# Kernel optimization log

Measured on AMD Instinct MI355X. Metric: run time of the kernel, lower is better.

## Reference

```python
import jax, jax.numpy as jnp
import numpy as np
from jax import lax

TAGSET = 9
START, STOP = 7, 8
HID = 500  # hidden_dim // 2 per direction
BERT_H = 768
T = 8192
NEG = -10000.0


def setup_inputs() -> dict:
    key = jax.random.key(0)
    ks = jax.random.split(key, 16)
    trans = jax.random.normal(ks[13], (TAGSET, TAGSET), jnp.float32)
    trans = trans.at[START, :].set(NEG).at[:, STOP].set(NEG)
    return {
        "embeddings": jax.random.normal(ks[0], (T, BERT_H), jnp.float32),
        "w_ih_f": jax.random.normal(ks[1], (4 * HID, BERT_H), jnp.float32) * 0.05,
        "w_hh_f": jax.random.normal(ks[2], (4 * HID, HID), jnp.float32) * 0.05,
        "b_ih_f": jax.random.normal(ks[3], (4 * HID,), jnp.float32) * 0.05,
        "b_hh_f": jax.random.normal(ks[4], (4 * HID,), jnp.float32) * 0.05,
        "w_ih_b": jax.random.normal(ks[5], (4 * HID, BERT_H), jnp.float32) * 0.05,
        "w_hh_b": jax.random.normal(ks[6], (4 * HID, HID), jnp.float32) * 0.05,
        "b_ih_b": jax.random.normal(ks[7], (4 * HID,), jnp.float32) * 0.05,
        "b_hh_b": jax.random.normal(ks[8], (4 * HID,), jnp.float32) * 0.05,
        "h0": jax.random.normal(ks[9], (2, HID), jnp.float32),
        "c0": jax.random.normal(ks[10], (2, HID), jnp.float32),
        "w_tag": jax.random.normal(ks[11], (TAGSET, 2 * HID), jnp.float32) * 0.05,
        "b_tag": jax.random.normal(ks[12], (TAGSET,), jnp.float32) * 0.05,
        "transitions": trans,
    }


def _lstm_dir(x, w_ih, w_hh, b_ih, b_hh, h0, c0, reverse):
    # pre-compute input projections for all timesteps: [T, 4H]
    xproj = x @ w_ih.T + b_ih + b_hh

    def step(carry, xp):
        h, c = carry
        g = xp + w_hh @ h  # [4H]
        i, f, gg, o = jnp.split(g, 4)  # torch gate order: i, f, g, o
        i, f, o = jax.nn.sigmoid(i), jax.nn.sigmoid(f), jax.nn.sigmoid(o)
        c = f * c + i * jnp.tanh(gg)
        h = o * jnp.tanh(c)
        return (h, c), h

    _, hs = lax.scan(step, (h0, c0), xproj, reverse=reverse)
    return hs  # [T, H]


def _viterbi(feats, transitions):
    init = jnp.full((TAGSET,), NEG, feats.dtype).at[START].set(0.0)

    def step(fv, feat):
        scores = fv[None, :] + transitions  # [next_tag, prev_tag]
        bptr = jnp.argmax(scores, axis=1)
        fv_new = jnp.max(scores, axis=1) + feat
        return fv_new, bptr

    fv, bptrs = lax.scan(step, init, feats)  # bptrs: [T, TAGSET]
    terminal = fv + transitions[STOP]
    best_last = jnp.argmax(terminal)
    path_score = terminal[best_last]

    def back(tag, bp):
        return bp[tag], tag  # emit tag at time t, carry tag at t-1

    _, path = lax.scan(back, best_last, bptrs, reverse=True)
    return path_score, path


def reference(embeddings, w_ih_f, w_hh_f, b_ih_f, b_hh_f,
              w_ih_b, w_hh_b, b_ih_b, b_hh_b,
              h0, c0, w_tag, b_tag, transitions):
    h_fwd = _lstm_dir(embeddings, w_ih_f, w_hh_f, b_ih_f, b_hh_f, h0[0], c0[0], False)
    h_bwd = _lstm_dir(embeddings, w_ih_b, w_hh_b, b_ih_b, b_hh_b, h0[1], c0[1], True)
    lstm_out = jnp.concatenate([h_fwd, h_bwd], axis=-1)  # [T, 1000]
    feats = lstm_out @ w_tag.T + b_tag  # [T, TAGSET]
    score, path = _viterbi(feats, transitions)
    return score, path
```

## Files before the change

### kernel.cpp

```cpp
#include <hip/hip_runtime.h>
#include <hip/hip_bf16.h>
#include <math.h>

constexpr int TSEQ = 8192;
constexpr int BH   = 768;
constexpr int HID  = 500;
constexpr int H4   = 2000;
constexpr int NTAG = 9;
constexpr int START_TAG = 7;
constexpr int STOP_TAG  = 8;
constexpr float NEGV = -10000.0f;

constexpr int NWG = 32;
constexpr int UPW = 16;

constexpr size_t XP_OFF = 0;
constexpr size_t XP_SZ  = (size_t)2 * TSEQ * H4;
constexpr size_t HS_OFF = XP_OFF + XP_SZ;
constexpr size_t HS_SZ  = (size_t)2 * TSEQ * HID;
constexpr size_t FT_OFF = HS_OFF + HS_SZ;
constexpr size_t FT_SZ  = (size_t)TSEQ * NTAG;
constexpr size_t BUF_OFF = FT_OFF + FT_SZ;

__device__ __forceinline__ float wave_reduce_sum(float v) {
    int x;
    x = __builtin_amdgcn_update_dpp(0, __float_as_int(v), 0x111, 0xF, 0xF, true);
    v += __int_as_float(x);
    x = __builtin_amdgcn_update_dpp(0, __float_as_int(v), 0x112, 0xF, 0xF, true);
    v += __int_as_float(x);
    x = __builtin_amdgcn_update_dpp(0, __float_as_int(v), 0x114, 0xF, 0xF, true);
    v += __int_as_float(x);
    x = __builtin_amdgcn_update_dpp(0, __float_as_int(v), 0x118, 0xF, 0xF, true);
    v += __int_as_float(x);
    x = __builtin_amdgcn_update_dpp(0, __float_as_int(v), 0x142, 0xF, 0xF, true);
    v += __int_as_float(x);
    x = __builtin_amdgcn_update_dpp(0, __float_as_int(v), 0x143, 0xF, 0xF, true);
    v += __int_as_float(x);
    return v;
}

__global__ __launch_bounds__(256) void xproj_gemm(
    const float* __restrict__ A,
    const float* __restrict__ Wf, const float* __restrict__ Wb,
    const float* __restrict__ bif, const float* __restrict__ bhf,
    const float* __restrict__ bib, const float* __restrict__ bhb,
    float* __restrict__ out)
{
    __shared__ __align__(16) float As[8 * 128];
    __shared__ __align__(16) float Bs[8 * 128];

    const int bx = blockIdx.x, by = blockIdx.y;
    const int d    = by >> 4;
    const int col0 = (by & 15) << 7;
    const int row0 = bx << 7;
    const float* W  = d ? Wb : Wf;
    const float* bi = d ? bib : bif;
    const float* bh = d ? bhb : bhf;

    const int tid = threadIdx.x;
    const int tx = tid & 15, ty = tid >> 4;

    float acc[8][8];
#pragma unroll
    for (int i = 0; i < 8; ++i)
#pragma unroll
        for (int j = 0; j < 8; ++j) acc[i][j] = 0.f;

    const int lm = tid >> 1;
    const int lk = (tid & 1) << 2;
    const float* Ap = A + (size_t)(row0 + lm) * BH + lk;
    const int wcol = col0 + lm;
    const bool wok = wcol < H4;
    const float* Wp = W + (size_t)(wok ? wcol : 0) * BH + lk;

    for (int k0 = 0; k0 < BH; k0 += 8) {
        const float4 av = *(const float4*)(Ap + k0);
        float4 bv = make_float4(0.f, 0.f, 0.f, 0.f);
        if (wok) bv = *(const float4*)(Wp + k0);
        __syncthreads();
        As[(lk + 0) * 128 + lm] = av.x;
        As[(lk + 1) * 128 + lm] = av.y;
        As[(lk + 2) * 128 + lm] = av.z;
        As[(lk + 3) * 128 + lm] = av.w;
        Bs[(lk + 0) * 128 + lm] = bv.x;
        Bs[(lk + 1) * 128 + lm] = bv.y;
        Bs[(lk + 2) * 128 + lm] = bv.z;
        Bs[(lk + 3) * 128 + lm] = bv.w;
        __syncthreads();
#pragma unroll
        for (int kk = 0; kk < 8; ++kk) {
            float a[8], b[8];
            *(float4*)&a[0] = *(const float4*)&As[kk * 128 + ty * 8];
            *(float4*)&a[4] = *(const float4*)&As[kk * 128 + ty * 8 + 4];
            *(float4*)&b[0] = *(const float4*)&Bs[kk * 128 + tx * 8];
            *(float4*)&b[4] = *(const float4*)&Bs[kk * 128 + tx * 8 + 4];
#pragma unroll
            for (int i = 0; i < 8; ++i)
#pragma unroll
                for (int j = 0; j < 8; ++j)
                    acc[i][j] = fmaf(a[i], b[j], acc[i][j]);
        }
    }

#pragma unroll
    for (int i = 0; i < 8; ++i) {
        const int r = row0 + ty * 8 + i;
#pragma unroll
        for (int j = 0; j < 8; ++j) {
            const int cc = col0 + tx * 8 + j;
            if (cc < H4)
                out[((size_t)d * TSEQ + r) * H4 + cc] = acc[i][j] + bi[cc] + bh[cc];
        }
    }
}

__global__ __launch_bounds__(512) void lstm_rec(
    const float* __restrict__ whhf, const float* __restrict__ whhb,
    const float* __restrict__ h0, const float* __restrict__ c0,
    const float* __restrict__ xproj_all, float* __restrict__ hseq_all,
    unsigned long long* bufbase)
{
    __shared__ __align__(16) float wlds[64 * 512];
    __shared__ __align__(16) float hs[512];
    __shared__ float gparts[64];

    const int bx = blockIdx.x;
    const int d = bx & 1, w = bx >> 1;
    const float* whh = d ? whhb : whhf;
    const float* xproj = xproj_all + (size_t)d * TSEQ * H4;
    float* hseq = hseq_all + (size_t)d * TSEQ * HID;
    unsigned long long* bufd = bufbase + d * 1024;

    const int j0 = w * UPW;
    int nu = HID - j0; if (nu > UPW) nu = UPW; if (nu < 0) nu = 0;
    const int tid = threadIdx.x, l = tid & 63, wv = tid >> 6;

    for (int idx = tid; idx < 64 * 512; idx += 512) {
        const int r = idx >> 9, c = idx & 511;
        const int g = r >> 4, u = r & 15;
        float vv = 0.f;
        if (c < HID && u < nu)
            vv = whh[(size_t)(g * HID + j0 + u) * HID + c];
        wlds[idx] = vv;
    }
    float creg = 0.f;
    if (tid < nu) {
        creg = c0[d * HID + j0 + tid];
        const unsigned long long pk =
            (unsigned long long)__float_as_uint(h0[d * HID + j0 + tid]);
        __hip_atomic_store(&bufd[j0 + tid], pk,
                           __ATOMIC_RELAXED, __HIP_MEMORY_SCOPE_AGENT);
    }
    __syncthreads();

    const int ua = 4 * l, ub = 256 + 4 * l;
    const bool gb0 = (ub + 0 >= HID), gb1 = (ub + 1 >= HID);
    const bool gb2 = (ub + 2 >= HID), gb3 = (ub + 3 >= HID);

    for (int step = 0; step < TSEQ; ++step) {
        const int t = d ? (TSEQ - 1 - step) : step;

        float xp0 = 0.f, xp1 = 0.f, xp2 = 0.f, xp3 = 0.f;
        if (tid < nu) {
            const float* xr = xproj + (size_t)t * H4 + j0 + tid;
            xp0 = xr[0]; xp1 = xr[HID]; xp2 = xr[2 * HID]; xp3 = xr[3 * HID];
        }

        if (wv == 0) {
            unsigned long long* bp = bufd + ((step & 1) << 9);
            const unsigned long long want = (unsigned long long)(unsigned)step;
            unsigned long long va0, va1, va2, va3, vb0, vb1, vb2, vb3;
            for (;;) {
                va0 = __hip_atomic_load(&bp[ua + 0], __ATOMIC_RELAXED, __HIP_MEMORY_SCOPE_AGENT);
                va1 = __hip_atomic_load(&bp[ua + 1], __ATOMIC_RELAXED, __HIP_MEMORY_SCOPE_AGENT);
                va2 = __hip_atomic_load(&bp[ua + 2], __ATOMIC_RELAXED, __HIP_MEMORY_SCOPE_AGENT);
                va3 = __hip_atomic_load(&bp[ua + 3], __ATOMIC_RELAXED, __HIP_MEMORY_SCOPE_AGENT);
                vb0 = __hip_atomic_load(&bp[ub + 0], __ATOMIC_RELAXED, __HIP_MEMORY_SCOPE_AGENT);
                vb1 = __hip_atomic_load(&bp[ub + 1], __ATOMIC_RELAXED, __HIP_MEMORY_SCOPE_AGENT);
                vb2 = __hip_atomic_load(&bp[ub + 2], __ATOMIC_RELAXED, __HIP_MEMORY_SCOPE_AGENT);
                vb3 = __hip_atomic_load(&bp[ub + 3], __ATOMIC_RELAXED, __HIP_MEMORY_SCOPE_AGENT);
                bool ok = true;
                ok &= ((va0 >> 32) == want);
                ok &= ((va1 >> 32) == want);
                ok &= ((va2 >> 32) == want);
                ok &= ((va3 >> 32) == want);
                ok &= gb0 || ((vb0 >> 32) == want);
                ok &= gb1 || ((vb1 >> 32) == want);
                ok &= gb2 || ((vb2 >> 32) == want);
                ok &= gb3 || ((vb3 >> 32) == want);
                if (__all(ok)) break;
            }
            float4 fa, fb;
            fa.x = __uint_as_float((unsigned)va0);
            fa.y = __uint_as_float((unsigned)va1);
            fa.z = __uint_as_float((unsigned)va2);
            fa.w = __uint_as_float((unsigned)va3);
            fb.x = __uint_as_float((unsigned)vb0);
            fb.y = __uint_as_float((unsigned)vb1);
            fb.z = __uint_as_float((unsigned)vb2);
            fb.w = __uint_as_float((unsigned)vb3);
            *(float4*)&hs[ua] = fa;
            *(float4*)&hs[ub] = fb;
        }
        __syncthreads();

        const float4 ha = *(const float4*)&hs[ua];
        const float4 hb = *(const float4*)&hs[ub];
#pragma unroll
        for (int r8 = 0; r8 < 8; ++r8) {
            const int row = (wv << 3) + r8;
            const float4 w0 = *(const float4*)&wlds[(row << 9) + ua];
            const float4 w1 = *(const float4*)&wlds[(row << 9) + ub];
            float p = w0.x * ha.x + w0.y * ha.y + w0.z * ha.z + w0.w * ha.w
                    + w1.x * hb.x + w1.y * hb.y + w1.z * hb.z + w1.w * hb.w;
            p = wave_reduce_sum(p);
            if (l == 63) gparts[row] = p;
        }
        __syncthreads();

        if (tid < nu) {
            const float gi = gparts[tid]      + xp0;
            const float gf = gparts[16 + tid] + xp1;
            const float gg = gparts[32 + tid] + xp2;
            const float go = gparts[48 + tid] + xp3;
            const float si = 1.f / (1.f + expf(-gi));
            const float sf = 1.f / (1.f + expf(-gf));
            const float so = 1.f / (1.f + expf(-go));
            const float c = sf * creg + si * tanhf(gg);
            creg = c;
            const float h = so * tanhf(c);
            const unsigned long long pk =
                ((unsigned long long)(unsigned)(step + 1) << 32) | __float_as_uint(h);
            __hip_atomic_store(&bufd[(((step + 1) & 1) << 9) + j0 + tid], pk,
                               __ATOMIC_RELAXED, __HIP_MEMORY_SCOPE_AGENT);
            hseq[(size_t)t * HID + j0 + tid] = h;
        }
    }
}

__global__ __launch_bounds__(256) void feats_kern(
    const float* __restrict__ hsf, const float* __restrict__ hsb,
    const float* __restrict__ wtag, const float* __restrict__ btag,
    float* __restrict__ feats)
{
    __shared__ float wt[NTAG * 1000];
    __shared__ float bt[NTAG];
    const int tid = threadIdx.x;
    for (int idx = tid; idx < NTAG * 1000; idx += 256) wt[idx] = wtag[idx];
    if (tid < NTAG) bt[tid] = btag[tid];
    __syncthreads();

    const int t = blockIdx.x * 4 + (tid >> 6);
    const int l = tid & 63;
    float acc[NTAG];
#pragma unroll
    for (int n = 0; n < NTAG; ++n) acc[n] = 0.f;

#pragma unroll
    for (int j = 0; j < 16; ++j) {
        const int k = l + 64 * j;
        if (k < 1000) {
            const float a = (k < HID) ? hsf[(size_t)t * HID + k]
                                      : hsb[(size_t)t * HID + k - HID];
#pragma unroll
            for (int n = 0; n < NTAG; ++n)
                acc[n] = fmaf(wt[n * 1000 + k], a, acc[n]);
        }
    }
#pragma unroll
    for (int n = 0; n < NTAG; ++n) {
        acc[n] += __shfl_xor(acc[n], 1, 64);
        acc[n] += __shfl_xor(acc[n], 2, 64);
        acc[n] += __shfl_xor(acc[n], 4, 64);
        acc[n] += __shfl_xor(acc[n], 8, 64);
        acc[n] += __shfl_xor(acc[n], 16, 64);
        acc[n] += __shfl_xor(acc[n], 32, 64);
    }
    if (l < NTAG) feats[(size_t)t * NTAG + l] = acc[l] + bt[l];
}

__global__ __launch_bounds__(256) void viterbi_kern(
    const float* __restrict__ feats, const float* __restrict__ trans,
    float* __restrict__ out)
{
    __shared__ unsigned char bp[TSEQ * NTAG];
    __shared__ float fch[512 * NTAG];
    __shared__ __align__(16) float fvL[12];
    __shared__ unsigned char amap[256];
    __shared__ unsigned char entry[32];
    __shared__ int s_best;

    const int tid = threadIdx.x, l = tid & 63, wv = tid >> 6;
    const int ln = (l < NTAG) ? l : NTAG - 1;
    float tr[NTAG];
#pragma unroll
    for (int p = 0; p < NTAG; ++p) tr[p] = trans[ln * NTAG + p];

    if (tid < 12) fvL[tid] = (tid == START_TAG) ? 0.f : NEGV;
    __syncthreads();

    for (int c = 0; c < 16; ++c) {
        for (int idx = tid; idx < 512 * NTAG; idx += 256)
            fch[idx] = feats[(size_t)c * 512 * NTAG + idx];
        __syncthreads();
        if (wv == 0) {
            for (int tt = 0; tt < 512; ++tt) {
                const float ft = fch[tt * NTAG + ln];
                const float4 f0 = *(const float4*)&fvL[0];
                const float4 f1 = *(const float4*)&fvL[4];
                const float f8 = fvL[8];
                const float c0 = f0.x + tr[0];
                const float c1 = f0.y + tr[1];
                const float c2 = f0.z + tr[2];
                const float c3 = f0.w + tr[3];
                const float c4 = f1.x + tr[4];
                const float c5 = f1.y + tr[5];
                const float c6 = f1.z + tr[6];
                const float c7 = f1.w + tr[7];
                const float c8 = f8   + tr[8];
                const float m0 = fmaxf(fmaxf(c0, c1), c2);
                const float m1 = fmaxf(fmaxf(c3, c4), c5);
                const float m2 = fmaxf(fmaxf(c6, c7), c8);
                const float best = fmaxf(fmaxf(m0, m1), m2);
                unsigned m = (c0 == best ? 1u : 0u)
                           | (c1 == best ? 2u : 0u)
                           | (c2 == best ? 4u : 0u)
                           | (c3 == best ? 8u : 0u)
                           | (c4 == best ? 16u : 0u)
                           | (c5 == best ? 32u : 0u)
                           | (c6 == best ? 64u : 0u)
                           | (c7 == best ? 128u : 0u)
                           | (c8 == best ? 256u : 0u);
                const int b = __builtin_ctz(m);
                const float nf = best + ft;
                if (l < NTAG) {
                    bp[(size_t)(c * 512 + tt) * NTAG + l] = (unsigned char)b;
                    fvL[l] = nf;
                }
            }
        }
        __syncthreads();
    }

    if (tid == 0) {
        float bestv = -3.0e38f; int bi = 0;
#pragma unroll
        for (int p = 0; p < NTAG; ++p) {
            const float s = fvL[p] + trans[STOP_TAG * NTAG + p];
            if (s > bestv) { bestv = s; bi = p; }
        }
        out[0] = bestv; s_best = bi;
    }
    __syncthreads();

    if (tid < 252) {
        const int ch = tid / 9, tg = tid % 9;
        const int s = ch * 293;
        const int e = (s + 293 < TSEQ) ? s + 293 : TSEQ;
        int tag = tg;
        for (int t = e - 1; t >= s; --t) tag = bp[t * NTAG + tag];
        amap[ch * 9 + tg] = (unsigned char)tag;
    }
    __syncthreads();
    if (tid == 0) {
        int tag = s_best;
        entry[27] = (unsigned char)tag;
        for (int ch = 27; ch >= 1; --ch) {
            tag = amap[ch * 9 + tag];
            entry[ch - 1] = (unsigned char)tag;
        }
    }
    __syncthreads();
    if (tid < 28) {
        const int ch = tid;
        const int s = ch * 293;
        const int e = (s + 293 < TSEQ) ? s + 293 : TSEQ;
        int tag = entry[ch];
        for (int t = e - 1; t >= s; --t) {
            out[1 + t] = (float)tag;
            tag = bp[t * NTAG + tag];
        }
    }
}

extern "C" void kernel_launch(void* const* d_in, const int* in_sizes, int n_in,
                              void* d_out, int out_size, void* d_ws, size_t ws_size,
                              hipStream_t stream) {
    const float* emb  = (const float*)d_in[0];
    const float* wihf = (const float*)d_in[1];
    const float* whhf = (const float*)d_in[2];
    const float* bihf = (const float*)d_in[3];
    const float* bhhf = (const float*)d_in[4];
    const float* wihb = (const float*)d_in[5];
    const float* whhb = (const float*)d_in[6];
    const float* bihb = (const float*)d_in[7];
    const float* bhhb = (const float*)d_in[8];
    const float* h0   = (const float*)d_in[9];
    const float* c0   = (const float*)d_in[10];
    const float* wtag = (const float*)d_in[11];
    const float* btag = (const float*)d_in[12];
    const float* trans = (const float*)d_in[13];

    float* ws = (float*)d_ws;
    float* out = (float*)d_out;

    xproj_gemm<<<dim3(64, 32), 256, 0, stream>>>(
        emb, wihf, wihb, bihf, bhhf, bihb, bhhb, ws + XP_OFF);

    lstm_rec<<<2 * NWG, 512, 0, stream>>>(
        whhf, whhb, h0, c0, ws + XP_OFF, ws + HS_OFF,
        (unsigned long long*)(ws + BUF_OFF));

    feats_kern<<<TSEQ / 4, 256, 0, stream>>>(
        ws + HS_OFF, ws + HS_OFF + (size_t)TSEQ * HID, wtag, btag, ws + FT_OFF);

    viterbi_kern<<<1, 256, 0, stream>>>(ws + FT_OFF, trans, out);
}
```

Measured before the change: 20.88 ms.

## Remove per-step block barriers in LSTM recurrence via wave-local gate ownership

```diff
diff --git a/kernel.cpp b/kernel.cpp
--- a/kernel.cpp
+++ b/kernel.cpp
@@ -121,8 +121,8 @@
     unsigned long long* bufbase)
 {
     __shared__ __align__(16) float wlds[64 * 512];
-    __shared__ __align__(16) float hs[512];
-    __shared__ float gparts[64];
+    __shared__ __align__(16) float hs[2][512];
+    __shared__ int seq;
 
     const int bx = blockIdx.x;
     const int d = bx & 1, w = bx >> 1;
@@ -136,22 +136,31 @@
     const int tid = threadIdx.x, l = tid & 63, wv = tid >> 6;
 
     for (int idx = tid; idx < 64 * 512; idx += 512) {
-        const int r = idx >> 9, c = idx & 511;
-        const int g = r >> 4, u = r & 15;
+        const int rr = idx >> 9, c = idx & 511;
+        const int wvr = rr >> 3, k = rr & 7;
+        const int u = 2 * wvr + (k & 1), g = k >> 1;
         float vv = 0.f;
         if (c < HID && u < nu)
             vv = whh[(size_t)(g * HID + j0 + u) * HID + c];
         wlds[idx] = vv;
     }
-    float creg = 0.f;
+    if (tid == 0) seq = 0;
+
+    const int uA = 2 * wv, uB = 2 * wv + 1;
+    const bool hA = uA < nu, hB = uB < nu;
+    float cAr = 0.f, cBr = 0.f;
+    if (l == 63) {
+        if (hA) cAr = c0[d * HID + j0 + uA];
+        if (hB) cBr = c0[d * HID + j0 + uB];
+    }
     if (tid < nu) {
-        creg = c0[d * HID + j0 + tid];
         const unsigned long long pk =
             (unsigned long long)__float_as_uint(h0[d * HID + j0 + tid]);
         __hip_atomic_store(&bufd[j0 + tid], pk,
                            __ATOMIC_RELAXED, __HIP_MEMORY_SCOPE_AGENT);
     }
     __syncthreads();
+    if (wv != 0 && !hA) return;
 
     const int ua = 4 * l, ub = 256 + 4 * l;
     const bool gb0 = (ub + 0 >= HID), gb1 = (ub + 1 >= HID);
@@ -160,12 +169,17 @@
     for (int step = 0; step < TSEQ; ++step) {
         const int t = d ? (TSEQ - 1 - step) : step;
 
-        float xp0 = 0.f, xp1 = 0.f, xp2 = 0.f, xp3 = 0.f;
-        if (tid < nu) {
-            const float* xr = xproj + (size_t)t * H4 + j0 + tid;
-            xp0 = xr[0]; xp1 = xr[HID]; xp2 = xr[2 * HID]; xp3 = xr[3 * HID];
-        }
-
+        float xA0 = 0.f, xA1 = 0.f, xA2 = 0.f, xA3 = 0.f;
+        float xB0 = 0.f, xB1 = 0.f, xB2 = 0.f, xB3 = 0.f;
+        if (l == 63) {
+            const float* xr = xproj + (size_t)t * H4 + j0;
+            if (hA) { xA0 = xr[uA]; xA1 = xr[HID + uA];
+                      xA2 = xr[2 * HID + uA]; xA3 = xr[3 * HID + uA]; }
+            if (hB) { xB0 = xr[uB]; xB1 = xr[HID + uB];
+                      xB2 = xr[2 * HID + uB]; xB3 = xr[3 * HID + uB]; }
+        }
+
+        float4 ha, hb;
         if (wv == 0) {
             unsigned long long* bp = bufd + ((step & 1) << 9);
             const unsigned long long want = (unsigned long long)(unsigned)step;
@@ -190,50 +204,71 @@
                 ok &= gb3 || ((vb3 >> 32) == want);
                 if (__all(ok)) break;
             }
-            float4 fa, fb;
-            fa.x = __uint_as_float((unsigned)va0);
-            fa.y = __uint_as_float((unsigned)va1);
-            fa.z = __uint_as_float((unsigned)va2);
-            fa.w = __uint_as_float((unsigned)va3);
-            fb.x = __uint_as_float((unsigned)vb0);
-            fb.y = __uint_as_float((unsigned)vb1);
-            fb.z = __uint_as_float((unsigned)vb2);
-            fb.w = __uint_as_float((unsigned)vb3);
-            *(float4*)&hs[ua] = fa;
-            *(float4*)&hs[ub] = fb;
-        }
-        __syncthreads();
-
-        const float4 ha = *(const float4*)&hs[ua];
-        const float4 hb = *(const float4*)&hs[ub];
-#pragma unroll
-        for (int r8 = 0; r8 < 8; ++r8) {
-            const int row = (wv << 3) + r8;
+            ha.x = __uint_as_float((unsigned)va0);
+            ha.y = __uint_as_float((unsigned)va1);
+            ha.z = __uint_as_float((unsigned)va2);
+            ha.w = __uint_as_float((unsigned)va3);
+            hb.x = __uint_as_float((unsigned)vb0);
+            hb.y = __uint_as_float((unsigned)vb1);
+            hb.z = __uint_as_float((unsigned)vb2);
+            hb.w = __uint_as_float((unsigned)vb3);
+            *(float4*)&hs[step & 1][ua] = ha;
+            *(float4*)&hs[step & 1][ub] = hb;
+            __hip_atomic_store(&seq, step + 1,
+                               __ATOMIC_RELEASE, __HIP_MEMORY_SCOPE_WORKGROUP);
+        } else {
+            while (__hip_atomic_load(&seq, __ATOMIC_ACQUIRE,
+                                     __HIP_MEMORY_SCOPE_WORKGROUP) < step + 1) {}
+            ha = *(const float4*)&hs[step & 1][ua];
+            hb = *(const float4*)&hs[step & 1][ub];
+        }
+
+        float sums[8];
+#pragma unroll
+        for (int k = 0; k < 8; ++k) {
+            const int row = (wv << 3) + k;
             const float4 w0 = *(const float4*)&wlds[(row << 9) + ua];
             const float4 w1 = *(const float4*)&wlds[(row << 9) + ub];
             float p = w0.x * ha.x + w0.y * ha.y + w0.z * ha.z + w0.w * ha.w
                     + w1.x * hb.x + w1.y * hb.y + w1.z * hb.z + w1.w * hb.w;
-            p = wave_reduce_sum(p);
-            if (l == 63) gparts[row] = p;
-        }
-        __syncthreads();
-
-        if (tid < nu) {
-            const float gi = gparts[tid]      + xp0;
-            const float gf = gparts[16 + tid] + xp1;
-            const float gg = gparts[32 + tid] + xp2;
-            const float go = gparts[48 + tid] + xp3;
-            const float si = 1.f / (1.f + expf(-gi));
-            const float sf = 1.f / (1.f + expf(-gf));
-            const float so = 1.f / (1.f + expf(-go));
-            const float c = sf * creg + si * tanhf(gg);
-            creg = c;
-            const float h = so * tanhf(c);
-            const unsigned long long pk =
-                ((unsigned long long)(unsigned)(step + 1) << 32) | __float_as_uint(h);
-            __hip_atomic_store(&bufd[(((step + 1) & 1) << 9) + j0 + tid], pk,
-                               __ATOMIC_RELAXED, __HIP_MEMORY_SCOPE_AGENT);
-            hseq[(size_t)t * HID + j0 + tid] = h;
+            sums[k] = wave_reduce_sum(p);
+        }
+
+        if (l == 63) {
+            if (hA) {
+                const float gi = sums[0] + xA0;
+                const float gf = sums[2] + xA1;
+                const float gg = sums[4] + xA2;
+                const float go = sums[6] + xA3;
+                const float si = 1.f / (1.f + expf(-gi));
+                const float sf = 1.f / (1.f + expf(-gf));
+                const float so = 1.f / (1.f + expf(-go));
+                const float c = sf * cAr + si * tanhf(gg);
+                cAr = c;
+                const float h = so * tanhf(c);
+                const unsigned long long pk =
+                    ((unsigned long long)(unsigned)(step + 1) << 32) | __float_as_uint(h);
+                __hip_atomic_store(&bufd[(((step + 1) & 1) << 9) + j0 + uA], pk,
+                                   __ATOMIC_RELAXED, __HIP_MEMORY_SCOPE_AGENT);
+                hseq[(size_t)t * HID + j0 + uA] = h;
+            }
+            if (hB) {
+                const float gi = sums[1] + xB0;
+                const float gf = sums[3] + xB1;
+                const float gg = sums[5] + xB2;
+                const float go = sums[7] + xB3;
+                const float si = 1.f / (1.f + expf(-gi));
+                const float sf = 1.f / (1.f + expf(-gf));
+                const float so = 1.f / (1.f + expf(-go));
+                const float c = sf * cBr + si * tanhf(gg);
+                cBr = c;
+                const float h = so * tanhf(c);
+                const unsigned long long pk =
+                    ((unsigned long long)(unsigned)(step + 1) << 32) | __float_as_uint(h);
+                __hip_atomic_store(&bufd[(((step + 1) & 1) << 9) + j0 + uB], pk,
+                                   __ATOMIC_RELAXED, __HIP_MEMORY_SCOPE_AGENT);
+                hseq[(size_t)t * HID + j0 + uB] = h;
+            }
         }
     }
 }
```

Measured after the change: 30.78 ms. 1.47x slower.
